# Kernel optimization log

Measured on AMD Instinct MI355X. Metric: run time of the kernel, lower is better.

The kernel has to match this reference:

```python
import jax, jax.numpy as jnp
import numpy as np

I = 6156  # input feature size
O = 3     # output classes
B = 2048  # batch


def setup_inputs() -> dict:
    key = jax.random.key(0)
    ks = jax.random.split(key, 6)
    x = jax.random.normal(ks[0], (B, I), dtype=jnp.float32)
    # nn.Linear(input_size, output_size)
    lin_w = jax.random.normal(ks[1], (O, I), dtype=jnp.float32) * (1.0 / np.sqrt(I))
    lin_b = jax.random.normal(ks[2], (O,), dtype=jnp.float32) * 0.01
    # interaction_weights: xavier_uniform_ on (I, I)
    limit = float(np.sqrt(6.0 / (I + I)))
    w_int = jax.random.uniform(ks[3], (I, I), dtype=jnp.float32, minval=-limit, maxval=limit)
    # final_layer: nn.Linear(I + O, O)
    fin_w = jax.random.normal(ks[4], (O, I + O), dtype=jnp.float32) * (1.0 / np.sqrt(I + O))
    fin_b = jax.random.normal(ks[5], (O,), dtype=jnp.float32) * 0.01
    return {"x": x, "lin_w": lin_w, "lin_b": lin_b, "w_int": w_int,
            "fin_w": fin_w, "fin_b": fin_b}


def reference(x, lin_w, lin_b, w_int, fin_w, fin_b):
    # linear_logits = x @ lin_w.T + lin_b  -> [B, O]
    linear_logits = x @ lin_w.T + lin_b
    # einsum('bi,bj,ij->bij').sum(dim=2) == x * (x @ w_int.T)
    # GEMM [B,I]x[I,I] + elementwise multiply; no O(B*I*I) intermediate.
    interactions = x * (x @ w_int.T)  # [B, I]
    combined = jnp.concatenate([linear_logits, interactions], axis=1)  # [B, O+I]
    logits = combined @ fin_w.T + fin_b  # [B, O]
    return logits
```

## Files before the change

### kernel.cpp

```cpp
#include <hip/hip_runtime.h>
#include <hip/hip_bf16.h>

constexpr int Bsz = 2048;
constexpr int Iin = 6156;
constexpr int IF  = 6159;
constexpr int Kp  = 6208;
constexpr int NpW = 6400;
constexpr int NTI = Kp / 64;
constexpr int MT  = Bsz / 256;
constexpr int NTN = 25;

typedef __attribute__((ext_vector_type(8))) short short8;
typedef __attribute__((ext_vector_type(4))) float f32x4;
typedef __attribute__((ext_vector_type(4))) int   i32x4;

#define AS1 __attribute__((address_space(1)))
#define AS3 __attribute__((address_space(3)))

__device__ __forceinline__ short f2bf(float f) {
    union { float f; unsigned u; } v; v.f = f;
    unsigned r = v.u + 0x7FFFu + ((v.u >> 16) & 1u);
    return (short)(r >> 16);
}

__device__ __forceinline__ short8 pack8(float4 a, float4 b) {
    short8 r;
    r[0] = f2bf(a.x); r[1] = f2bf(a.y); r[2] = f2bf(a.z); r[3] = f2bf(a.w);
    r[4] = f2bf(b.x); r[5] = f2bf(b.y); r[6] = f2bf(b.z); r[7] = f2bf(b.w);
    return r;
}

__device__ __forceinline__ void stage_chunk(const void* src, const void* ldsbase) {
    __builtin_amdgcn_global_load_lds((const AS1 void*)src, (AS3 void*)ldsbase, 16, 0, 0);
}

__global__ void linear_init_kernel(const float* __restrict__ x,
                                   const float* __restrict__ lin_w,
                                   const float* __restrict__ lin_b,
                                   const float* __restrict__ fin_w,
                                   const float* __restrict__ fin_b,
                                   float* __restrict__ out) {
    int wid  = threadIdx.x >> 6;
    int lane = threadIdx.x & 63;
    int b = blockIdx.x * 4 + wid;
    if (b >= Bsz) return;
    const float4* xr = (const float4*)(x + (size_t)b * Iin);
    const float4* w0 = (const float4*)(lin_w);
    const float4* w1 = (const float4*)(lin_w + Iin);
    const float4* w2 = (const float4*)(lin_w + 2 * Iin);
    float s0 = 0.f, s1 = 0.f, s2 = 0.f;
    for (int i = lane; i < Iin / 4; i += 64) {
        float4 xv = xr[i];
        float4 a0 = w0[i], a1 = w1[i], a2 = w2[i];
        s0 += xv.x * a0.x + xv.y * a0.y + xv.z * a0.z + xv.w * a0.w;
        s1 += xv.x * a1.x + xv.y * a1.y + xv.z * a1.z + xv.w * a1.w;
        s2 += xv.x * a2.x + xv.y * a2.y + xv.z * a2.z + xv.w * a2.w;
    }
    #pragma unroll
    for (int off = 1; off < 64; off <<= 1) {
        s0 += __shfl_xor(s0, off, 64);
        s1 += __shfl_xor(s1, off, 64);
        s2 += __shfl_xor(s2, off, 64);
    }
    if (lane == 0) {
        float l0 = s0 + lin_b[0], l1 = s1 + lin_b[1], l2 = s2 + lin_b[2];
        #pragma unroll
        for (int o = 0; o < 3; ++o) {
            out[b * 3 + o] = fin_b[o]
                + fin_w[(size_t)o * IF + 0] * l0
                + fin_w[(size_t)o * IF + 1] * l1
                + fin_w[(size_t)o * IF + 2] * l2;
        }
    }
}

__global__ __launch_bounds__(256) void quant_kernel(
    const float* __restrict__ src, signed char* __restrict__ dst,
    float* __restrict__ scales, int src_rows) {
    __shared__ float rowbuf[Kp];
    __shared__ float red[4];
    int row = blockIdx.x;
    int t   = threadIdx.x;
    float amax = 0.f;
    if (row < src_rows) {
        const float4* s = (const float4*)(src + (size_t)row * Iin);
        for (int i = t; i < Iin / 4; i += 256) {
            float4 v = s[i];
            ((float4*)rowbuf)[i] = v;
            amax = fmaxf(amax, fmaxf(fmaxf(fabsf(v.x), fabsf(v.y)),
                                     fmaxf(fabsf(v.z), fabsf(v.w))));
        }
        for (int i = Iin + t; i < Kp; i += 256) rowbuf[i] = 0.f;
    } else {
        for (int i = t; i < Kp; i += 256) rowbuf[i] = 0.f;
    }
    #pragma unroll
    for (int off = 1; off < 64; off <<= 1)
        amax = fmaxf(amax, __shfl_xor(amax, off, 64));
    if ((t & 63) == 0) red[t >> 6] = amax;
    __syncthreads();
    float am = fmaxf(fmaxf(red[0], red[1]), fmaxf(red[2], red[3]));
    float rs = (am > 0.f) ? 127.f / am : 0.f;
    if (t == 0) scales[row] = (am > 0.f) ? am / 127.f : 0.f;

    int xorv = (row >> 1) & 3;
    for (int p = t; p < Kp / 16; p += 256) {
        int blk = p >> 2, sub = p & 3;
        int sc  = (blk << 6) + ((sub ^ xorv) << 4);
        i32x4 pk;
        #pragma unroll
        for (int j = 0; j < 4; ++j) {
            unsigned u = 0;
            #pragma unroll
            for (int e = 0; e < 4; ++e) {
                float v = rowbuf[sc + j * 4 + e] * rs;
                int q = (int)rintf(v);
                q = q > 127 ? 127 : (q < -127 ? -127 : q);
                u |= ((unsigned)(q & 255)) << (8 * e);
            }
            pk[j] = (int)u;
        }
        *(i32x4*)(dst + (size_t)row * Kp + (size_t)p * 16) = pk;
    }
}

__global__ __launch_bounds__(512, 2) void gemm_i8(
    const signed char* __restrict__ xq, const signed char* __restrict__ wq,
    const float* __restrict__ sx, const float* __restrict__ sw,
    const float* __restrict__ xf, const float* __restrict__ finw,
    float* __restrict__ out) {

    __shared__ signed char lsA[4][16384];
    __shared__ signed char lsB[4][16384];
    __shared__ float part[256][3];

    const int tid  = threadIdx.x;
    const int lane = tid & 63;
    const int wid  = tid >> 6;
    const int wr   = wid >> 2;
    const int wc   = wid & 3;
    const int l15  = lane & 15;
    const int koff = (((lane >> 4) ^ ((lane >> 1) & 3)) << 4);

    int swz = ((int)blockIdx.x & 7) * NTN + ((int)blockIdx.x >> 3);
    int tm = swz & 7;
    int tn = swz >> 3;
    int bm0 = tm << 8;
    int in0 = tn << 8;

    i32x4 acc[8][4];
    #pragma unroll
    for (int m = 0; m < 8; ++m)
        #pragma unroll
        for (int n = 0; n < 4; ++n)
            acc[m][n] = (i32x4){0, 0, 0, 0};

    auto stageA = [&](int tk, int h) {
        int idx = h * 512 + tid;
        int row = idx >> 2, sub = idx & 3;
        const signed char* src = xq + (size_t)(bm0 + row) * Kp + tk * 64 + sub * 16;
        stage_chunk(src, &lsA[tk & 3][(size_t)idx * 16]);
    };
    auto stageB = [&](int tk, int h) {
        int idx = h * 512 + tid;
        int row = idx >> 2, sub = idx & 3;
        const signed char* src = wq + (size_t)(in0 + row) * Kp + tk * 64 + sub * 16;
        stage_chunk(src, &lsB[tk & 3][(size_t)idx * 16]);
    };
    auto ldA = [&](int slot, int m) -> i32x4 {
        int row = wr * 128 + m * 16 + l15;
        return *(const i32x4*)&lsA[slot][row * 64 + koff];
    };
    auto ldB = [&](int slot, int n) -> i32x4 {
        int row = wc * 64 + n * 16 + l15;
        return *(const i32x4*)&lsB[slot][row * 64 + koff];
    };

    i32x4 afA[8], afB[8], bf[4];

    stageA(0, 0); stageA(0, 1); stageB(0, 0); stageB(0, 1);
    stageA(1, 0); stageA(1, 1); stageB(1, 0); stageB(1, 1);
    stageA(2, 0); stageA(2, 1); stageB(2, 0); stageB(2, 1);
    asm volatile("s_waitcnt vmcnt(8)" ::: "memory");
    __builtin_amdgcn_s_barrier();
    #pragma unroll
    for (int m = 0; m < 8; ++m) afA[m] = ldA(0, m);

#define SEC(T, CUR, NXT, TW, DO_PF, DO_ST)                                \
    {                                                                     \
        asm volatile("s_waitcnt " TW ::: "memory");                       \
        __builtin_amdgcn_s_barrier();                                     \
        const int _sl = (T) & 3;                                          \
        _Pragma("unroll")                                                 \
        for (int n = 0; n < 4; ++n) bf[n] = ldB(_sl, n);                  \
        __builtin_amdgcn_sched_barrier(0);                                \
        if (DO_PF) {                                                      \
            const int _ns = ((T) + 1) & 3;                                \
            _Pragma("unroll")                                             \
            for (int m = 0; m < 8; ++m) NXT[m] = ldA(_ns, m);             \
        }                                                                 \
        __builtin_amdgcn_sched_barrier(0);                                \
        if (DO_ST) {                                                      \
            stageA((T) + 3, 0); stageA((T) + 3, 1);                       \
            stageB((T) + 3, 0); stageB((T) + 3, 1);                       \
        }                                                                 \
        __builtin_amdgcn_sched_barrier(0);                                \
        if (DO_PF) { asm volatile("s_waitcnt lgkmcnt(8)" ::: "memory"); } \
        else       { asm volatile("s_waitcnt lgkmcnt(0)" ::: "memory"); } \
        __builtin_amdgcn_sched_barrier(0);                                \
        __builtin_amdgcn_s_setprio(1);                                    \
        _Pragma("unroll")                                                 \
        for (int m = 0; m < 8; ++m)                                       \
            _Pragma("unroll")                                             \
            for (int n = 0; n < 4; ++n)                                   \
                acc[m][n] = __builtin_amdgcn_mfma_i32_16x16x64_i8(        \
                    CUR[m], bf[n], acc[m][n], 0, 0, 0);                   \
        __builtin_amdgcn_s_setprio(0);                                    \
        __builtin_amdgcn_sched_barrier(0);                                \
    }

    for (int i = 0; i < 47; ++i) {
        int t = 2 * i;
        SEC(t,     afA, afB, "vmcnt(4)", true, true);
        SEC(t + 1, afB, afA, "vmcnt(4)", true, true);
    }
    SEC(94, afA, afB, "vmcnt(4)", true,  false);
    SEC(95, afB, afA, "vmcnt(0)", true,  false);
    SEC(96, afA, afB, "vmcnt(0)", false, false);
#undef SEC

    __syncthreads();
    for (int t = tid; t < 768; t += 512) ((float*)part)[t] = 0.f;
    __syncthreads();

    int q4 = lane >> 4;
    #pragma unroll
    for (int m = 0; m < 8; ++m) {
        #pragma unroll
        for (int r = 0; r < 4; ++r) {
            int lr = wr * 128 + m * 16 + q4 * 4 + r;
            int bg = bm0 + lr;
            float sxv = sx[bg];
            float s0 = 0.f, s1 = 0.f, s2 = 0.f;
            #pragma unroll
            for (int n = 0; n < 4; ++n) {
                int gi = in0 + wc * 64 + n * 16 + l15;
                if (gi < Iin) {
                    float z = (float)acc[m][n][r] * sxv * sw[gi];
                    float inter = z * xf[(size_t)bg * Iin + gi];
                    s0 += inter * finw[(size_t)0 * IF + 3 + gi];
                    s1 += inter * finw[(size_t)1 * IF + 3 + gi];
                    s2 += inter * finw[(size_t)2 * IF + 3 + gi];
                }
            }
            #pragma unroll
            for (int off = 1; off < 16; off <<= 1) {
                s0 += __shfl_xor(s0, off, 64);
                s1 += __shfl_xor(s1, off, 64);
                s2 += __shfl_xor(s2, off, 64);
            }
            if (l15 == 0) {
                atomicAdd(&part[lr][0], s0);
                atomicAdd(&part[lr][1], s1);
                atomicAdd(&part[lr][2], s2);
            }
        }
    }
    __syncthreads();
    for (int t = tid; t < 768; t += 512) {
        int lr = t / 3, o = t - lr * 3;
        atomicAdd(&out[(size_t)(bm0 + lr) * 3 + o], part[lr][o]);
    }
}

__global__ __launch_bounds__(256) void gemm_fallback(
    const float* __restrict__ xf, const float* __restrict__ wf,
    const float* __restrict__ finw, float* __restrict__ out) {

    __shared__ short lsA[128 * 64];
    __shared__ short lsB[128 * 64];
    __shared__ float part[128][3];

    int tid  = threadIdx.x;
    int lane = tid & 63;
    int wid  = tid >> 6;
    int wm   = wid & 1;
    int wn   = wid >> 1;

    int ntiles = (Bsz / 128) * (6272 / 128);
    int tile = (blockIdx.x & 7) * (ntiles >> 3) + (blockIdx.x >> 3);
    int tm = tile & 15;
    int tn = tile >> 4;
    int bm0 = tm << 7;
    int in0 = tn << 7;

    f32x4 acc[4][4];
    #pragma unroll
    for (int m = 0; m < 4; ++m)
        #pragma unroll
        for (int n = 0; n < 4; ++n)
            acc[m][n] = (f32x4){0.f, 0.f, 0.f, 0.f};

    for (int k0 = 0; k0 < Kp; k0 += 64) {
        #pragma unroll
        for (int it = 0; it < 4; ++it) {
            int idx = it * 256 + tid;
            int r   = idx >> 3;
            int seg = idx & 7;
            int kc  = k0 + seg * 8;
            int sd  = (seg ^ (r & 7)) << 3;
            {
                const float* s = xf + (size_t)(bm0 + r) * Iin + kc;
                short8 st;
                if (kc + 8 <= Iin) {
                    float4 f0 = *(const float4*)s;
                    float4 f1 = *(const float4*)(s + 4);
                    st = pack8(f0, f1);
                } else {
                    #pragma unroll
                    for (int e = 0; e < 8; ++e) {
                        float v = (kc + e < Iin) ? s[e] : 0.f;
                        st[e] = f2bf(v);
                    }
                }
                *(short8*)&lsA[r * 64 + sd] = st;
            }
            {
                int grow = in0 + r;
                short8 st;
                if (grow < Iin && kc + 8 <= Iin) {
                    const float* s = wf + (size_t)grow * Iin + kc;
                    float4 f0 = *(const float4*)s;
                    float4 f1 = *(const float4*)(s + 4);
                    st = pack8(f0, f1);
                } else if (grow < Iin) {
                    const float* s = wf + (size_t)grow * Iin + kc;
                    #pragma unroll
                    for (int e = 0; e < 8; ++e) {
                        float v = (kc + e < Iin) ? s[e] : 0.f;
                        st[e] = f2bf(v);
                    }
                } else {
                    #pragma unroll
                    for (int e = 0; e < 8; ++e) st[e] = 0;
                }
                *(short8*)&lsB[r * 64 + sd] = st;
            }
        }
        __syncthreads();

        #pragma unroll
        for (int kk = 0; kk < 2; ++kk) {
            int q = (kk << 2) + (lane >> 4);
            short8 af[4], bfr[4];
            #pragma unroll
            for (int m = 0; m < 4; ++m) {
                int R = wm * 64 + m * 16 + (lane & 15);
                af[m] = *(const short8*)&lsA[R * 64 + ((q ^ (R & 7)) << 3)];
            }
            #pragma unroll
            for (int n = 0; n < 4; ++n) {
                int R = wn * 64 + n * 16 + (lane & 15);
                bfr[n] = *(const short8*)&lsB[R * 64 + ((q ^ (R & 7)) << 3)];
            }
            #pragma unroll
            for (int m = 0; m < 4; ++m)
                #pragma unroll
                for (int n = 0; n < 4; ++n)
                    acc[m][n] = __builtin_amdgcn_mfma_f32_16x16x32_bf16(
                        af[m], bfr[n], acc[m][n], 0, 0, 0);
        }
        __syncthreads();
    }

    for (int t = tid; t < 384; t += 256) ((float*)part)[t] = 0.f;
    __syncthreads();

    #pragma unroll
    for (int m = 0; m < 4; ++m) {
        int rowbase = bm0 + wm * 64 + m * 16 + ((lane >> 4) << 2);
        #pragma unroll
        for (int r = 0; r < 4; ++r) {
            int b = rowbase + r;
            float s0 = 0.f, s1 = 0.f, s2 = 0.f;
            #pragma unroll
            for (int n = 0; n < 4; ++n) {
                int gi = in0 + wn * 64 + n * 16 + (lane & 15);
                if (gi < Iin) {
                    float inter = acc[m][n][r] * xf[(size_t)b * Iin + gi];
                    s0 += inter * finw[(size_t)0 * IF + 3 + gi];
                    s1 += inter * finw[(size_t)1 * IF + 3 + gi];
                    s2 += inter * finw[(size_t)2 * IF + 3 + gi];
                }
            }
            #pragma unroll
            for (int off = 1; off < 16; off <<= 1) {
                s0 += __shfl_xor(s0, off, 64);
                s1 += __shfl_xor(s1, off, 64);
                s2 += __shfl_xor(s2, off, 64);
            }
            if ((lane & 15) == 0) {
                int lr = b - bm0;
                atomicAdd(&part[lr][0], s0);
                atomicAdd(&part[lr][1], s1);
                atomicAdd(&part[lr][2], s2);
            }
        }
    }
    __syncthreads();
    for (int t = tid; t < 384; t += 256) {
        int lr = t / 3, o = t - lr * 3;
        atomicAdd(&out[(size_t)(bm0 + lr) * 3 + o], part[lr][o]);
    }
}

extern "C" void kernel_launch(void* const* d_in, const int* in_sizes, int n_in,
                              void* d_out, int out_size, void* d_ws, size_t ws_size,
                              hipStream_t stream) {
    const float* x     = (const float*)d_in[0];
    const float* lin_w = (const float*)d_in[1];
    const float* lin_b = (const float*)d_in[2];
    const float* w_int = (const float*)d_in[3];
    const float* fin_w = (const float*)d_in[4];
    const float* fin_b = (const float*)d_in[5];
    float* out = (float*)d_out;

    linear_init_kernel<<<Bsz / 4, 256, 0, stream>>>(x, lin_w, lin_b, fin_w, fin_b, out);

    const size_t xq_bytes = (size_t)Bsz * Kp;
    const size_t wq_bytes = (size_t)NpW * Kp;
    const size_t sx_off   = xq_bytes + wq_bytes;
    const size_t need = sx_off + (Bsz + NpW) * sizeof(float);

    if (ws_size >= need) {
        signed char* xq = (signed char*)d_ws;
        signed char* wq = xq + xq_bytes;
        float* sxp = (float*)((char*)d_ws + sx_off);
        float* swp = sxp + Bsz;
        quant_kernel<<<Bsz, 256, 0, stream>>>(x, xq, sxp, Bsz);
        quant_kernel<<<NpW, 256, 0, stream>>>(w_int, wq, swp, Iin);
        gemm_i8<<<MT * NTN, 512, 0, stream>>>(xq, wq, sxp, swp, x, fin_w, out);
    } else {
        const int ntiles = (Bsz / 128) * (6272 / 128);
        gemm_fallback<<<ntiles, 256, 0, stream>>>(x, w_int, fin_w, out);
    }
}
```

Measured before the change: 175.7 us.

## Shrink int8 GEMM tile to 256x128 with simple double-buffered loop

Replaces the 256x256 block tile with a 256x128 tile, doubling the grid to 400 blocks and allowing up to four blocks per CU via smaller LDS buffers (2-stage instead of 4-stage). The hand-scheduled software pipeline with register prefetch of A fragments is replaced by a plain loop that waits for all loads, stages the next tile, then loads fragments and issues MFMAs. The aim is better occupancy and CU load balance across 256 CUs, at the cost of less data reuse per block, more global traffic for the x tiles, and less latency hiding within a wave. The block-index swizzle for L2 locality is also dropped.

```diff
diff --git a/kernel.cpp b/kernel.cpp
--- a/kernel.cpp
+++ b/kernel.cpp
@@ -7,8 +7,6 @@
 constexpr int Kp  = 6208;
 constexpr int NpW = 6400;
 constexpr int NTI = Kp / 64;
-constexpr int MT  = Bsz / 256;
-constexpr int NTN = 25;
 
 typedef __attribute__((ext_vector_type(8))) short short8;
 typedef __attribute__((ext_vector_type(4))) float f32x4;
@@ -124,51 +122,52 @@
     }
 }
 
-__global__ __launch_bounds__(512, 2) void gemm_i8(
+__global__ __launch_bounds__(512, 4) void gemm_i8t(
     const signed char* __restrict__ xq, const signed char* __restrict__ wq,
     const float* __restrict__ sx, const float* __restrict__ sw,
     const float* __restrict__ xf, const float* __restrict__ finw,
     float* __restrict__ out) {
 
-    __shared__ signed char lsA[4][16384];
-    __shared__ signed char lsB[4][16384];
+    __shared__ signed char lsA[2][16384];
+    __shared__ signed char lsB[2][8192];
     __shared__ float part[256][3];
 
     const int tid  = threadIdx.x;
     const int lane = tid & 63;
     const int wid  = tid >> 6;
-    const int wr   = wid >> 2;
-    const int wc   = wid & 3;
+    const int wr   = wid >> 1;
+    const int wc   = wid & 1;
     const int l15  = lane & 15;
     const int koff = (((lane >> 4) ^ ((lane >> 1) & 3)) << 4);
 
-    int swz = ((int)blockIdx.x & 7) * NTN + ((int)blockIdx.x >> 3);
-    int tm = swz & 7;
-    int tn = swz >> 3;
-    int bm0 = tm << 8;
-    int in0 = tn << 8;
-
-    i32x4 acc[8][4];
-    #pragma unroll
-    for (int m = 0; m < 8; ++m)
+    const int tm = (int)blockIdx.x & 7;
+    const int tn = (int)blockIdx.x >> 3;
+    const int bm0 = tm << 8;
+    const int in0 = tn << 7;
+
+    i32x4 acc[4][4];
+    #pragma unroll
+    for (int m = 0; m < 4; ++m)
         #pragma unroll
         for (int n = 0; n < 4; ++n)
             acc[m][n] = (i32x4){0, 0, 0, 0};
 
-    auto stageA = [&](int tk, int h) {
-        int idx = h * 512 + tid;
-        int row = idx >> 2, sub = idx & 3;
-        const signed char* src = xq + (size_t)(bm0 + row) * Kp + tk * 64 + sub * 16;
-        stage_chunk(src, &lsA[tk & 3][(size_t)idx * 16]);
+    auto stageA = [&](int tk) {
+        #pragma unroll
+        for (int j = 0; j < 2; ++j) {
+            int idx = j * 512 + tid;
+            int row = idx >> 2, sub = idx & 3;
+            const signed char* src = xq + (size_t)(bm0 + row) * Kp + tk * 64 + sub * 16;
+            stage_chunk(src, &lsA[tk & 1][(size_t)idx * 16]);
+        }
     };
-    auto stageB = [&](int tk, int h) {
-        int idx = h * 512 + tid;
-        int row = idx >> 2, sub = idx & 3;
+    auto stageB = [&](int tk) {
+        int row = tid >> 2, sub = tid & 3;
         const signed char* src = wq + (size_t)(in0 + row) * Kp + tk * 64 + sub * 16;
-        stage_chunk(src, &lsB[tk & 3][(size_t)idx * 16]);
+        stage_chunk(src, &lsB[tk & 1][(size_t)tid * 16]);
     };
     auto ldA = [&](int slot, int m) -> i32x4 {
-        int row = wr * 128 + m * 16 + l15;
+        int row = wr * 64 + m * 16 + l15;
         return *(const i32x4*)&lsA[slot][row * 64 + koff];
     };
     auto ldB = [&](int slot, int n) -> i32x4 {
@@ -176,58 +175,28 @@
         return *(const i32x4*)&lsB[slot][row * 64 + koff];
     };
 
-    i32x4 afA[8], afB[8], bf[4];
-
-    stageA(0, 0); stageA(0, 1); stageB(0, 0); stageB(0, 1);
-    stageA(1, 0); stageA(1, 1); stageB(1, 0); stageB(1, 1);
-    stageA(2, 0); stageA(2, 1); stageB(2, 0); stageB(2, 1);
-    asm volatile("s_waitcnt vmcnt(8)" ::: "memory");
-    __builtin_amdgcn_s_barrier();
-    #pragma unroll
-    for (int m = 0; m < 8; ++m) afA[m] = ldA(0, m);
-
-#define SEC(T, CUR, NXT, TW, DO_PF, DO_ST)                                \
-    {                                                                     \
-        asm volatile("s_waitcnt " TW ::: "memory");                       \
-        __builtin_amdgcn_s_barrier();                                     \
-        const int _sl = (T) & 3;                                          \
-        _Pragma("unroll")                                                 \
-        for (int n = 0; n < 4; ++n) bf[n] = ldB(_sl, n);                  \
-        __builtin_amdgcn_sched_barrier(0);                                \
-        if (DO_PF) {                                                      \
-            const int _ns = ((T) + 1) & 3;                                \
-            _Pragma("unroll")                                             \
-            for (int m = 0; m < 8; ++m) NXT[m] = ldA(_ns, m);             \
-        }                                                                 \
-        __builtin_amdgcn_sched_barrier(0);                                \
-        if (DO_ST) {                                                      \
-            stageA((T) + 3, 0); stageA((T) + 3, 1);                       \
-            stageB((T) + 3, 0); stageB((T) + 3, 1);                       \
-        }                                                                 \
-        __builtin_amdgcn_sched_barrier(0);                                \
-        if (DO_PF) { asm volatile("s_waitcnt lgkmcnt(8)" ::: "memory"); } \
-        else       { asm volatile("s_waitcnt lgkmcnt(0)" ::: "memory"); } \
-        __builtin_amdgcn_sched_barrier(0);                                \
-        __builtin_amdgcn_s_setprio(1);                                    \
-        _Pragma("unroll")                                                 \
-        for (int m = 0; m < 8; ++m)                                       \
-            _Pragma("unroll")                                             \
-            for (int n = 0; n < 4; ++n)                                   \
-                acc[m][n] = __builtin_amdgcn_mfma_i32_16x16x64_i8(        \
-                    CUR[m], bf[n], acc[m][n], 0, 0, 0);                   \
-        __builtin_amdgcn_s_setprio(0);                                    \
-        __builtin_amdgcn_sched_barrier(0);                                \
-    }
-
-    for (int i = 0; i < 47; ++i) {
-        int t = 2 * i;
-        SEC(t,     afA, afB, "vmcnt(4)", true, true);
-        SEC(t + 1, afB, afA, "vmcnt(4)", true, true);
-    }
-    SEC(94, afA, afB, "vmcnt(4)", true,  false);
-    SEC(95, afB, afA, "vmcnt(0)", true,  false);
-    SEC(96, afA, afB, "vmcnt(0)", false, false);
-#undef SEC
+    stageA(0); stageB(0);
+
+    for (int t = 0; t < NTI; ++t) {
+        asm volatile("s_waitcnt vmcnt(0)" ::: "memory");
+        __builtin_amdgcn_s_barrier();
+        __builtin_amdgcn_sched_barrier(0);
+        if (t + 1 < NTI) { stageA(t + 1); stageB(t + 1); }
+        __builtin_amdgcn_sched_barrier(0);
+
+        const int sl = t & 1;
+        i32x4 af[4], bf[4];
+        #pragma unroll
+        for (int m = 0; m < 4; ++m) af[m] = ldA(sl, m);
+        #pragma unroll
+        for (int n = 0; n < 4; ++n) bf[n] = ldB(sl, n);
+        #pragma unroll
+        for (int m = 0; m < 4; ++m)
+            #pragma unroll
+            for (int n = 0; n < 4; ++n)
+                acc[m][n] = __builtin_amdgcn_mfma_i32_16x16x64_i8(
+                    af[m], bf[n], acc[m][n], 0, 0, 0);
+    }
 
     __syncthreads();
     for (int t = tid; t < 768; t += 512) ((float*)part)[t] = 0.f;
@@ -235,10 +204,10 @@
 
     int q4 = lane >> 4;
     #pragma unroll
-    for (int m = 0; m < 8; ++m) {
+    for (int m = 0; m < 4; ++m) {
         #pragma unroll
         for (int r = 0; r < 4; ++r) {
-            int lr = wr * 128 + m * 16 + q4 * 4 + r;
+            int lr = wr * 64 + m * 16 + q4 * 4 + r;
             int bg = bm0 + lr;
             float sxv = sx[bg];
             float s0 = 0.f, s1 = 0.f, s2 = 0.f;
@@ -439,7 +408,7 @@
         float* swp = sxp + Bsz;
         quant_kernel<<<Bsz, 256, 0, stream>>>(x, xq, sxp, Bsz);
         quant_kernel<<<NpW, 256, 0, stream>>>(w_int, wq, swp, Iin);
-        gemm_i8<<<MT * NTN, 512, 0, stream>>>(xq, wq, sxp, swp, x, fin_w, out);
+        gemm_i8t<<<8 * 50, 512, 0, stream>>>(xq, wq, sxp, swp, x, fin_w, out);
     } else {
         const int ntiles = (Bsz / 128) * (6272 / 128);
         gemm_fallback<<<ntiles, 256, 0, stream>>>(x, w_int, fin_w, out);
```

Result: slower. 181.5 us (+3.3%).
